# Optimization experiments

Hardware: AMD Instinct MI355X
Metric: run time of the kernel (lower is better)

Reference implementation:

```python
import jax, jax.numpy as jnp
import numpy as np

B, S, D_MODEL = 4, 1024, 1024
HEADS, D_KEY, D_VAL = 16, 64, 64


def setup_inputs() -> dict:
    key = jax.random.key(0)
    ks = jax.random.split(key, 8)
    # glorot-ish scaled params
    sk = 1.0 / np.sqrt(D_MODEL)
    X = jax.random.normal(ks[0], (B, S, D_MODEL), dtype=jnp.float32)
    Wk = jax.random.normal(ks[1], (HEADS, D_MODEL, D_KEY), dtype=jnp.float32) * sk
    Wq = jax.random.normal(ks[2], (HEADS, D_MODEL, D_KEY), dtype=jnp.float32) * sk
    Wv = jax.random.normal(ks[3], (HEADS, D_MODEL, D_VAL), dtype=jnp.float32) * sk
    bk = jnp.zeros((HEADS, D_KEY), dtype=jnp.float32)
    bq = jnp.zeros((HEADS, D_KEY), dtype=jnp.float32)
    bv = jnp.zeros((HEADS, D_VAL), dtype=jnp.float32)
    Wo = jax.random.normal(ks[4], (HEADS * D_VAL, D_MODEL), dtype=jnp.float32) * (1.0 / np.sqrt(HEADS * D_VAL))
    bo = jnp.zeros((D_MODEL,), dtype=jnp.float32)
    return {"X": X, "Wk": Wk, "bk": bk, "Wq": Wq, "bq": bq, "Wv": Wv, "bv": bv, "Wo": Wo, "bo": bo}


def reference(X, Wk, bk, Wq, bq, Wv, bv, Wo, bo):
    # Per-head projections, batched over heads (original loops in Python)
    K = jnp.einsum('bsd,hdk->bhsk', X, Wk) + bk[None, :, None, :]
    Q = jnp.einsum('bsd,hdk->bhsk', X, Wq) + bq[None, :, None, :]
    V = jnp.einsum('bsd,hdv->bhsv', X, Wv) + bv[None, :, None, :]
    d_k = K.shape[-1]
    scores = jnp.einsum('bhqk,bhsk->bhqs', Q, K) / jnp.sqrt(jnp.asarray(d_k, X.dtype))
    A = jax.nn.softmax(scores, axis=-1)           # [B,H,S,S]
    Z = jnp.einsum('bhqs,bhsv->bhqv', A, V)        # [B,H,S,Dv]
    # concat heads: [B,S,H*Dv]
    Zc = jnp.transpose(Z, (0, 2, 1, 3)).reshape(X.shape[0], X.shape[1], -1)
    # output projection + residual; dropout is identity at inference
    return Zc @ Wo + bo + X
```

## Files before the change

kernel.cpp:

```cpp
#include <hip/hip_runtime.h>
#include <hip/hip_bf16.h>

typedef __bf16 bf16x8 __attribute__((ext_vector_type(8)));
typedef float f32x4 __attribute__((ext_vector_type(4)));
typedef unsigned short u16;
typedef u16 u16x4 __attribute__((ext_vector_type(4)));
typedef u16 u16x8 __attribute__((ext_vector_type(8)));
typedef short s16x4 __attribute__((ext_vector_type(4)));

#define LDA 72

__device__ inline u16 f2bf(float f) {
    union { float f; unsigned u; } v; v.f = f;
    unsigned r = v.u + 0x7fffu + ((v.u >> 16) & 1u);
    return (u16)(r >> 16);
}

#define GLD16(g, l) __builtin_amdgcn_global_load_lds( \
    (const __attribute__((address_space(1))) unsigned int*)(g), \
    (__attribute__((address_space(3))) unsigned int*)(l), 16, 0, 0)

__global__ void k_prep(const float* __restrict__ X, u16* __restrict__ Xb,
                       const float* __restrict__ Wk, const float* __restrict__ Wq,
                       const float* __restrict__ Wv, u16* __restrict__ WT,
                       const float* __restrict__ Wo, u16* __restrict__ WoT) {
    __shared__ u16 Ls[64 * LDA];
    int u = blockIdx.x, tid = threadIdx.x;
    if (u < 4096) {
        int idx = u * 256 + tid;
        float4 v = *(const float4*)&X[(size_t)idx * 4];
        u16x4 o; o.x = f2bf(v.x); o.y = f2bf(v.y); o.z = f2bf(v.z); o.w = f2bf(v.w);
        *(u16x4*)&Xb[(size_t)idx * 4] = o;
    } else if (u < 4864) {
        int b2 = u - 4096;
        int dt = b2 & 15, h = (b2 >> 4) & 15, p = b2 >> 8;
        const float* src = (p == 0 ? Wk : p == 1 ? Wq : Wv);
        int r0 = tid >> 4, c4 = tid & 15;
        for (int j = 0; j < 4; j++) {
            int d = r0 + j * 16;
            float4 v = *(const float4*)&src[((size_t)h * 1024 + dt * 64 + d) * 64 + c4 * 4];
            u16* q = &Ls[d * LDA + c4 * 4];
            q[0] = f2bf(v.x); q[1] = f2bf(v.y); q[2] = f2bf(v.z); q[3] = f2bf(v.w);
        }
        __syncthreads();
        int nk = tid >> 2, cd = tid & 3;
        u16 tmp[16];
        for (int j = 0; j < 16; j++) tmp[j] = Ls[(cd * 16 + j) * LDA + nk];
        size_t o = ((size_t)(p * 1024 + h * 64 + nk)) * 1024 + dt * 64 + cd * 16;
        *(u16x8*)&WT[o] = *(u16x8*)&tmp[0];
        *(u16x8*)&WT[o + 8] = *(u16x8*)&tmp[8];
    } else {
        int b2 = u - 4864;
        int dt = b2 & 15, nt2 = b2 >> 4;
        int r0 = tid >> 4, c4 = tid & 15;
        for (int j = 0; j < 4; j++) {
            int d = r0 + j * 16;
            float4 v = *(const float4*)&Wo[(size_t)(dt * 64 + d) * 1024 + nt2 * 64 + c4 * 4];
            u16* q = &Ls[d * LDA + c4 * 4];
            q[0] = f2bf(v.x); q[1] = f2bf(v.y); q[2] = f2bf(v.z); q[3] = f2bf(v.w);
        }
        __syncthreads();
        int nr = tid >> 2, cd = tid & 3;
        u16 tmp[16];
        for (int j = 0; j < 16; j++) tmp[j] = Ls[(cd * 16 + j) * LDA + nr];
        size_t o = ((size_t)(nt2 * 64 + nr)) * 1024 + dt * 64 + cd * 16;
        *(u16x8*)&WoT[o] = *(u16x8*)&tmp[0];
        *(u16x8*)&WoT[o + 8] = *(u16x8*)&tmp[8];
    }
}

__global__ __launch_bounds__(256, 3) void k_qkv(
    const u16* __restrict__ Xb, const u16* __restrict__ WT,
    const float* __restrict__ bk, const float* __restrict__ bq, const float* __restrict__ bv,
    u16* __restrict__ Kw, u16* __restrict__ Qw, u16* __restrict__ Vtw)
{
    __shared__ u16 As[128 * 64];
    __shared__ u16 Bs[128 * 64];
    int tid = threadIdx.x, w = tid >> 6, lane = tid & 63, quad = lane >> 4, l16 = lane & 15;
    int wm = w & 1, wn = w >> 1;
    int m0 = blockIdx.x * 128, n0 = blockIdx.y * 128;
    int rl = lane >> 3, ch = lane & 7, swch = ch ^ rl;
    const u16* Ag = Xb + (size_t)(m0 + w * 32 + rl) * 1024 + swch * 8;
    const u16* Bg = WT + (size_t)(n0 + w * 32 + rl) * 1024 + swch * 8;

    int hb = blockIdx.y * 2 + wn;
    int p = hb >> 4, hh = hb & 15;
    bool ct = (p < 2);

    f32x4 acc[4][4] = {};
    for (int k0 = 0; k0 < 1024; k0 += 64) {
        for (int i = 0; i < 4; i++) {
            GLD16(Ag + (size_t)i * 8 * 1024 + k0, &As[(w * 32 + i * 8) * 64]);
            GLD16(Bg + (size_t)i * 8 * 1024 + k0, &Bs[(w * 32 + i * 8) * 64]);
        }
        __syncthreads();
        for (int ks = 0; ks < 2; ks++) {
            bf16x8 af[4], bf[4];
            int c = (ks << 2) | quad;
            for (int mt = 0; mt < 4; mt++) {
                int row = wm * 64 + mt * 16 + l16;
                af[mt] = *(bf16x8*)&As[row * 64 + (c ^ (row & 7)) * 8];
            }
            for (int nt = 0; nt < 4; nt++) {
                int row = wn * 64 + nt * 16 + l16;
                bf[nt] = *(bf16x8*)&Bs[row * 64 + (c ^ (row & 7)) * 8];
            }
            if (ct) {
                for (int mt = 0; mt < 4; mt++)
                    for (int nt = 0; nt < 4; nt++)
                        acc[mt][nt] = __builtin_amdgcn_mfma_f32_16x16x32_bf16(bf[nt], af[mt], acc[mt][nt], 0, 0, 0);
            } else {
                for (int mt = 0; mt < 4; mt++)
                    for (int nt = 0; nt < 4; nt++)
                        acc[mt][nt] = __builtin_amdgcn_mfma_f32_16x16x32_bf16(af[mt], bf[nt], acc[mt][nt], 0, 0, 0);
            }
        }
        __syncthreads();
    }
    const float* bias = (p == 0 ? bk : p == 1 ? bq : bv) + hh * 64;
    if (ct) {
        u16* dst = (p == 0) ? Kw : Qw;
        float sc = (p == 0) ? 0.125f : 1.0f;
        for (int mt = 0; mt < 4; mt++) {
            int m = m0 + wm * 64 + mt * 16 + l16;
            int b = m >> 10, s = m & 1023;
            size_t base = ((size_t)((b << 4) + hh) * 1024 + s) * 64;
            for (int nt = 0; nt < 4; nt++) {
                float4 bb = *(const float4*)&bias[nt * 16 + quad * 4];
                u16x4 o;
                o[0] = f2bf((acc[mt][nt][0] + bb.x) * sc);
                o[1] = f2bf((acc[mt][nt][1] + bb.y) * sc);
                o[2] = f2bf((acc[mt][nt][2] + bb.z) * sc);
                o[3] = f2bf((acc[mt][nt][3] + bb.w) * sc);
                *(u16x4*)&dst[base + nt * 16 + quad * 4] = o;
            }
        }
    } else {
        for (int mt = 0; mt < 4; mt++)
            for (int nt = 0; nt < 4; nt++) {
                int nk = nt * 16 + l16;
                float bb = bias[nk];
                int mb = m0 + wm * 64 + mt * 16 + quad * 4;
                int b = mb >> 10, s = mb & 1023;
                u16x4 o;
                for (int r = 0; r < 4; r++) o[r] = f2bf(acc[mt][nt][r] + bb);
                *(u16x4*)&Vtw[((size_t)((b << 4) + hh) * 64 + nk) * 1024 + s] = o;
            }
    }
}

__global__ __launch_bounds__(512) void k_attn(
    const u16* __restrict__ Qw, const u16* __restrict__ Kw,
    const u16* __restrict__ Vtw, u16* __restrict__ Zw)
{
    __shared__ u16 Ks[2][64 * 64];
    __shared__ u16 Vs[2][64 * 64];
    int tid = threadIdx.x, w = tid >> 6, lane = tid & 63, quad = lane >> 4, l16 = lane & 15;
    int bh = blockIdx.x, q0 = blockIdx.y * 128;
    const u16* Qp = Qw + (size_t)bh * 65536;
    int rl = lane >> 3, ch = lane & 7, swch = ch ^ rl;
    const u16* Kg = Kw + (size_t)bh * 65536 + (w * 8 + rl) * 64 + swch * 8;
    const u16* Vg = Vtw + (size_t)bh * 65536 + (size_t)(w * 8 + rl) * 1024 + swch * 8;

    bf16x8 aq[2];
    for (int ks = 0; ks < 2; ks++)
        aq[ks] = *(const bf16x8*)&Qp[(size_t)(q0 + w * 16 + l16) * 64 + ks * 32 + quad * 8];

    f32x4 accT[4] = {};
    float accs_l = 0.f;

#define STAGE(st, buf) { int s0_ = (st) * 64; \
    GLD16(Kg + s0_ * 64, &Ks[buf][(w * 8) * 64]); \
    GLD16(Vg + s0_, &Vs[buf][(w * 8) * 64]); }

    STAGE(0, 0);
    for (int st = 0; st < 16; st++) {
        int buf = st & 1;
        __syncthreads();
        if (st < 15) STAGE(st + 1, buf ^ 1);
        f32x4 sacc[4] = {};
        __builtin_amdgcn_s_setprio(1);
        for (int ks = 0; ks < 2; ks++) {
            int c = (ks << 2) | quad;
            for (int nt = 0; nt < 4; nt++) {
                int row = nt * 16 + l16;
                bf16x8 kf = *(bf16x8*)&Ks[buf][row * 64 + (c ^ (row & 7)) * 8];
                sacc[nt] = __builtin_amdgcn_mfma_f32_16x16x32_bf16(kf, aq[ks], sacc[nt], 0, 0, 0);
            }
        }
        __builtin_amdgcn_s_setprio(0);
        s16x4 pb[4];
        for (int nt = 0; nt < 4; nt++)
            for (int r = 0; r < 4; r++) {
                float p = __builtin_exp2f(__builtin_fmaf(sacc[nt][r], 1.44269504f, -23.0831206f));
                accs_l += p;
                union { float f; unsigned u; } cv; cv.f = p;
                pb[nt][r] = (short)((cv.u + 0x8000u) >> 16);
            }
        __builtin_amdgcn_s_setprio(1);
        for (int nt = 0; nt < 4; nt++) {
            int sc = nt * 2 + (quad >> 1);
            for (int db = 0; db < 4; db++) {
                int row = db * 16 + l16;
                s16x4 vf = *(const s16x4*)&Vs[buf][row * 64 + ((sc ^ (row & 7)) << 3) + ((quad & 1) << 2)];
                accT[db] = __builtin_amdgcn_mfma_f32_16x16x16bf16_1k(vf, pb[nt], accT[db], 0, 0, 0);
            }
        }
        __builtin_amdgcn_s_setprio(0);
    }
#undef STAGE
    accs_l += __shfl_xor(accs_l, 16, 64);
    accs_l += __shfl_xor(accs_l, 32, 64);
    float inv = 1.f / accs_l;
    int b = bh >> 4, h = bh & 15;
    int q = q0 + w * 16 + l16;
    size_t base = ((size_t)(b * 1024 + q)) * 1024 + h * 64;
    for (int db = 0; db < 4; db++) {
        u16x4 o;
        for (int r = 0; r < 4; r++) o[r] = f2bf(accT[db][r] * inv);
        *(u16x4*)&Zw[base + db * 16 + quad * 4] = o;
    }
}

__global__ __launch_bounds__(256) void k_oproj(
    const u16* __restrict__ Zw, const u16* __restrict__ WoT, const float* __restrict__ bo,
    const float* __restrict__ X, float* __restrict__ out)
{
    __shared__ u16 As[64 * 64];
    __shared__ u16 Bs[128 * 64];
    int tid = threadIdx.x, w = tid >> 6, lane = tid & 63, quad = lane >> 4, l16 = lane & 15;
    int wm = w & 1, wn = w >> 1;
    int m0 = blockIdx.x * 64, n0 = blockIdx.y * 128;
    int rl = lane >> 3, ch = lane & 7, swch = ch ^ rl;
    const u16* Ag = Zw + (size_t)(m0 + w * 16 + rl) * 1024 + swch * 8;
    const u16* Bg = WoT + (size_t)(n0 + w * 32 + rl) * 1024 + swch * 8;

    f32x4 acc[2][4] = {};
    for (int k0 = 0; k0 < 1024; k0 += 64) {
        for (int i = 0; i < 2; i++)
            GLD16(Ag + (size_t)i * 8 * 1024 + k0, &As[(w * 16 + i * 8) * 64]);
        for (int i = 0; i < 4; i++)
            GLD16(Bg + (size_t)i * 8 * 1024 + k0, &Bs[(w * 32 + i * 8) * 64]);
        __syncthreads();
        for (int ks = 0; ks < 2; ks++) {
            bf16x8 af[2], bf[4];
            int c = (ks << 2) | quad;
            for (int mt = 0; mt < 2; mt++) {
                int row = wm * 32 + mt * 16 + l16;
                af[mt] = *(bf16x8*)&As[row * 64 + (c ^ (row & 7)) * 8];
            }
            for (int nt = 0; nt < 4; nt++) {
                int row = wn * 64 + nt * 16 + l16;
                bf[nt] = *(bf16x8*)&Bs[row * 64 + (c ^ (row & 7)) * 8];
            }
            for (int mt = 0; mt < 2; mt++)
                for (int nt = 0; nt < 4; nt++)
                    acc[mt][nt] = __builtin_amdgcn_mfma_f32_16x16x32_bf16(af[mt], bf[nt], acc[mt][nt], 0, 0, 0);
        }
        __syncthreads();
    }
    for (int mt = 0; mt < 2; mt++)
        for (int nt = 0; nt < 4; nt++) {
            int n = n0 + wn * 64 + nt * 16 + l16;
            float bb = bo[n];
            for (int r = 0; r < 4; r++) {
                int m = m0 + wm * 32 + mt * 16 + quad * 4 + r;
                out[(size_t)m * 1024 + n] = acc[mt][nt][r] + bb + X[(size_t)m * 1024 + n];
            }
        }
}

extern "C" void kernel_launch(void* const* d_in, const int* in_sizes, int n_in,
                              void* d_out, int out_size, void* d_ws, size_t ws_size,
                              hipStream_t stream) {
    const float* X  = (const float*)d_in[0];
    const float* Wk = (const float*)d_in[1];
    const float* bk = (const float*)d_in[2];
    const float* Wq = (const float*)d_in[3];
    const float* bq = (const float*)d_in[4];
    const float* Wv = (const float*)d_in[5];
    const float* bv = (const float*)d_in[6];
    const float* Wo = (const float*)d_in[7];
    const float* bo = (const float*)d_in[8];
    u16* ws = (u16*)d_ws;
    const size_t NQ = 4u * 16u * 1024u * 64u;
    u16* Qw  = ws;
    u16* Kw  = ws + NQ;
    u16* Vtw = ws + 2 * NQ;
    u16* Zw  = ws + 3 * NQ;
    u16* WT  = ws + 4 * NQ;
    u16* WoT = WT + 3 * 1048576;
    u16* Xb  = WoT + 1048576;
    float* outp = (float*)d_out;

    k_prep <<<5120, 256, 0, stream>>>(X, Xb, Wk, Wq, Wv, WT, Wo, WoT);
    k_qkv  <<<dim3(32, 24), 256, 0, stream>>>(Xb, WT, bk, bq, bv, Kw, Qw, Vtw);
    k_attn <<<dim3(64, 8), 512, 0, stream>>>(Qw, Kw, Vtw, Zw);
    k_oproj<<<dim3(64, 8), 256, 0, stream>>>(Zw, WoT, bo, X, outp);
}
```

Measured before the change: 180.8 us.

## Double-buffer LDS tiles in QKV and output-projection GEMMs

Both GEMM kernels now keep two LDS buffers and issue the global-to-LDS loads for the next k-tile before computing on the current one, with one barrier per iteration instead of two. The aim is to hide global load latency behind MFMA work. In exchange LDS use doubles (64KB per block for k_qkv), and launch bounds for k_qkv drop from 3 to 2 blocks per CU, which lowers occupancy. The single barrier before issuing the next loads into the other buffer appears to keep the scheme race-free.

```diff
diff --git a/kernel.cpp b/kernel.cpp
--- a/kernel.cpp
+++ b/kernel.cpp
@@ -69,13 +69,13 @@
     }
 }
 
-__global__ __launch_bounds__(256, 3) void k_qkv(
+__global__ __launch_bounds__(256, 2) void k_qkv(
     const u16* __restrict__ Xb, const u16* __restrict__ WT,
     const float* __restrict__ bk, const float* __restrict__ bq, const float* __restrict__ bv,
     u16* __restrict__ Kw, u16* __restrict__ Qw, u16* __restrict__ Vtw)
 {
-    __shared__ u16 As[128 * 64];
-    __shared__ u16 Bs[128 * 64];
+    __shared__ u16 As[2][128 * 64];
+    __shared__ u16 Bs[2][128 * 64];
     int tid = threadIdx.x, w = tid >> 6, lane = tid & 63, quad = lane >> 4, l16 = lane & 15;
     int wm = w & 1, wn = w >> 1;
     int m0 = blockIdx.x * 128, n0 = blockIdx.y * 128;
@@ -87,23 +87,26 @@
     int p = hb >> 4, hh = hb & 15;
     bool ct = (p < 2);
 
+#define QSTAGE(k0, b) for (int i = 0; i < 4; i++) { \
+        GLD16(Ag + (size_t)i * 8 * 1024 + (k0), &As[b][(w * 32 + i * 8) * 64]); \
+        GLD16(Bg + (size_t)i * 8 * 1024 + (k0), &Bs[b][(w * 32 + i * 8) * 64]); }
+
     f32x4 acc[4][4] = {};
-    for (int k0 = 0; k0 < 1024; k0 += 64) {
-        for (int i = 0; i < 4; i++) {
-            GLD16(Ag + (size_t)i * 8 * 1024 + k0, &As[(w * 32 + i * 8) * 64]);
-            GLD16(Bg + (size_t)i * 8 * 1024 + k0, &Bs[(w * 32 + i * 8) * 64]);
-        }
-        __syncthreads();
+    QSTAGE(0, 0);
+    for (int kk = 0; kk < 16; kk++) {
+        int buf = kk & 1;
+        __syncthreads();
+        if (kk < 15) QSTAGE((kk + 1) * 64, buf ^ 1);
         for (int ks = 0; ks < 2; ks++) {
             bf16x8 af[4], bf[4];
             int c = (ks << 2) | quad;
             for (int mt = 0; mt < 4; mt++) {
                 int row = wm * 64 + mt * 16 + l16;
-                af[mt] = *(bf16x8*)&As[row * 64 + (c ^ (row & 7)) * 8];
+                af[mt] = *(bf16x8*)&As[buf][row * 64 + (c ^ (row & 7)) * 8];
             }
             for (int nt = 0; nt < 4; nt++) {
                 int row = wn * 64 + nt * 16 + l16;
-                bf[nt] = *(bf16x8*)&Bs[row * 64 + (c ^ (row & 7)) * 8];
+                bf[nt] = *(bf16x8*)&Bs[buf][row * 64 + (c ^ (row & 7)) * 8];
             }
             if (ct) {
                 for (int mt = 0; mt < 4; mt++)
@@ -115,8 +118,8 @@
                         acc[mt][nt] = __builtin_amdgcn_mfma_f32_16x16x32_bf16(af[mt], bf[nt], acc[mt][nt], 0, 0, 0);
             }
         }
-        __syncthreads();
-    }
+    }
+#undef QSTAGE
     const float* bias = (p == 0 ? bk : p == 1 ? bq : bv) + hh * 64;
     if (ct) {
         u16* dst = (p == 0) ? Kw : Qw;
@@ -226,8 +229,8 @@
     const u16* __restrict__ Zw, const u16* __restrict__ WoT, const float* __restrict__ bo,
     const float* __restrict__ X, float* __restrict__ out)
 {
-    __shared__ u16 As[64 * 64];
-    __shared__ u16 Bs[128 * 64];
+    __shared__ u16 As[2][64 * 64];
+    __shared__ u16 Bs[2][128 * 64];
     int tid = threadIdx.x, w = tid >> 6, lane = tid & 63, quad = lane >> 4, l16 = lane & 15;
     int wm = w & 1, wn = w >> 1;
     int m0 = blockIdx.x * 64, n0 = blockIdx.y * 128;
@@ -235,30 +238,35 @@
     const u16* Ag = Zw + (size_t)(m0 + w * 16 + rl) * 1024 + swch * 8;
     const u16* Bg = WoT + (size_t)(n0 + w * 32 + rl) * 1024 + swch * 8;
 
+#define OSTAGE(k0, b) { \
+    for (int i = 0; i < 2; i++) \
+        GLD16(Ag + (size_t)i * 8 * 1024 + (k0), &As[b][(w * 16 + i * 8) * 64]); \
+    for (int i = 0; i < 4; i++) \
+        GLD16(Bg + (size_t)i * 8 * 1024 + (k0), &Bs[b][(w * 32 + i * 8) * 64]); }
+
     f32x4 acc[2][4] = {};
-    for (int k0 = 0; k0 < 1024; k0 += 64) {
-        for (int i = 0; i < 2; i++)
-            GLD16(Ag + (size_t)i * 8 * 1024 + k0, &As[(w * 16 + i * 8) * 64]);
-        for (int i = 0; i < 4; i++)
-            GLD16(Bg + (size_t)i * 8 * 1024 + k0, &Bs[(w * 32 + i * 8) * 64]);
-        __syncthreads();
+    OSTAGE(0, 0);
+    for (int kk = 0; kk < 16; kk++) {
+        int buf = kk & 1;
+        __syncthreads();
+        if (kk < 15) OSTAGE((kk + 1) * 64, buf ^ 1);
         for (int ks = 0; ks < 2; ks++) {
             bf16x8 af[2], bf[4];
             int c = (ks << 2) | quad;
             for (int mt = 0; mt < 2; mt++) {
                 int row = wm * 32 + mt * 16 + l16;
-                af[mt] = *(bf16x8*)&As[row * 64 + (c ^ (row & 7)) * 8];
+                af[mt] = *(bf16x8*)&As[buf][row * 64 + (c ^ (row & 7)) * 8];
             }
             for (int nt = 0; nt < 4; nt++) {
                 int row = wn * 64 + nt * 16 + l16;
-                bf[nt] = *(bf16x8*)&Bs[row * 64 + (c ^ (row & 7)) * 8];
+                bf[nt] = *(bf16x8*)&Bs[buf][row * 64 + (c ^ (row & 7)) * 8];
             }
             for (int mt = 0; mt < 2; mt++)
                 for (int nt = 0; nt < 4; nt++)
                     acc[mt][nt] = __builtin_amdgcn_mfma_f32_16x16x32_bf16(af[mt], bf[nt], acc[mt][nt], 0, 0, 0);
         }
-        __syncthreads();
-    }
+    }
+#undef OSTAGE
     for (int mt = 0; mt < 2; mt++)
         for (int nt = 0; nt < 4; nt++) {
             int n = n0 + wn * 64 + nt * 16 + l16;
```

After: 185.3 us. 1.02x slower.

## Load QKV GEMM operands directly from global memory, dropping LDS staging

Applied to the files above, without the earlier changes.

The QKV projection GEMM no longer stages X and weight tiles through shared memory with global_load_lds and barriers. Each wave now reads its MFMA fragments straight from global memory into registers. This removes the LDS traffic and both __syncthreads per k-step, and it drops the occupancy hint from launch_bounds. In exchange, tiles shared between waves are read from global memory more than once, and the small per-lane reads rely on caches to keep bandwidth reasonable.

```diff
diff --git a/kernel.cpp b/kernel.cpp
--- a/kernel.cpp
+++ b/kernel.cpp
@@ -69,53 +69,49 @@
     }
 }
 
-__global__ __launch_bounds__(256, 3) void k_qkv(
+__global__ __launch_bounds__(256) void k_qkv(
     const u16* __restrict__ Xb, const u16* __restrict__ WT,
     const float* __restrict__ bk, const float* __restrict__ bq, const float* __restrict__ bv,
     u16* __restrict__ Kw, u16* __restrict__ Qw, u16* __restrict__ Vtw)
 {
-    __shared__ u16 As[128 * 64];
-    __shared__ u16 Bs[128 * 64];
     int tid = threadIdx.x, w = tid >> 6, lane = tid & 63, quad = lane >> 4, l16 = lane & 15;
     int wm = w & 1, wn = w >> 1;
     int m0 = blockIdx.x * 128, n0 = blockIdx.y * 128;
-    int rl = lane >> 3, ch = lane & 7, swch = ch ^ rl;
-    const u16* Ag = Xb + (size_t)(m0 + w * 32 + rl) * 1024 + swch * 8;
-    const u16* Bg = WT + (size_t)(n0 + w * 32 + rl) * 1024 + swch * 8;
 
     int hb = blockIdx.y * 2 + wn;
     int p = hb >> 4, hh = hb & 15;
     bool ct = (p < 2);
 
+    const u16* Ap = Xb + (size_t)(m0 + wm * 64 + l16) * 1024 + quad * 8;
+    const u16* Bp = WT + (size_t)(n0 + wn * 64 + l16) * 1024 + quad * 8;
+
     f32x4 acc[4][4] = {};
+    #pragma unroll 1
     for (int k0 = 0; k0 < 1024; k0 += 64) {
-        for (int i = 0; i < 4; i++) {
-            GLD16(Ag + (size_t)i * 8 * 1024 + k0, &As[(w * 32 + i * 8) * 64]);
-            GLD16(Bg + (size_t)i * 8 * 1024 + k0, &Bs[(w * 32 + i * 8) * 64]);
-        }
-        __syncthreads();
+        #pragma unroll
         for (int ks = 0; ks < 2; ks++) {
             bf16x8 af[4], bf[4];
-            int c = (ks << 2) | quad;
-            for (int mt = 0; mt < 4; mt++) {
-                int row = wm * 64 + mt * 16 + l16;
-                af[mt] = *(bf16x8*)&As[row * 64 + (c ^ (row & 7)) * 8];
-            }
-            for (int nt = 0; nt < 4; nt++) {
-                int row = wn * 64 + nt * 16 + l16;
-                bf[nt] = *(bf16x8*)&Bs[row * 64 + (c ^ (row & 7)) * 8];
-            }
+            int kc = k0 + ks * 32;
+            #pragma unroll
+            for (int mt = 0; mt < 4; mt++)
+                af[mt] = *(const bf16x8*)&Ap[(size_t)mt * 16384 + kc];
+            #pragma unroll
+            for (int nt = 0; nt < 4; nt++)
+                bf[nt] = *(const bf16x8*)&Bp[(size_t)nt * 16384 + kc];
             if (ct) {
+                #pragma unroll
                 for (int mt = 0; mt < 4; mt++)
+                    #pragma unroll
                     for (int nt = 0; nt < 4; nt++)
                         acc[mt][nt] = __builtin_amdgcn_mfma_f32_16x16x32_bf16(bf[nt], af[mt], acc[mt][nt], 0, 0, 0);
             } else {
+                #pragma unroll
                 for (int mt = 0; mt < 4; mt++)
+                    #pragma unroll
                     for (int nt = 0; nt < 4; nt++)
                         acc[mt][nt] = __builtin_amdgcn_mfma_f32_16x16x32_bf16(af[mt], bf[nt], acc[mt][nt], 0, 0, 0);
             }
         }
-        __syncthreads();
     }
     const float* bias = (p == 0 ? bk : p == 1 ? bq : bv) + hh * 64;
     if (ct) {
```

After: 234.9 us. 29.9% more time.

## Double-buffer LDS tiles in QKV projection GEMM to overlap loads with MFMA

Applied to the files above, without the earlier changes.

The QKV projection kernel now uses two LDS buffers for the A and B tiles. It issues the global-to-LDS loads for the next K-step before computing on the current one, and waits with explicit vmcnt counts and raw barriers. The goal is to hide global load latency behind MFMA work instead of stalling on a full sync each iteration. LDS use doubles to 64KB per block and the occupancy hint of 3 is removed, so fewer blocks may be resident per CU.

```diff
diff --git a/kernel.cpp b/kernel.cpp
--- a/kernel.cpp
+++ b/kernel.cpp
@@ -69,13 +69,13 @@
     }
 }
 
-__global__ __launch_bounds__(256, 3) void k_qkv(
+__global__ __launch_bounds__(256) void k_qkv(
     const u16* __restrict__ Xb, const u16* __restrict__ WT,
     const float* __restrict__ bk, const float* __restrict__ bq, const float* __restrict__ bv,
     u16* __restrict__ Kw, u16* __restrict__ Qw, u16* __restrict__ Vtw)
 {
-    __shared__ u16 As[128 * 64];
-    __shared__ u16 Bs[128 * 64];
+    __shared__ u16 As[2][128 * 64];
+    __shared__ u16 Bs[2][128 * 64];
     int tid = threadIdx.x, w = tid >> 6, lane = tid & 63, quad = lane >> 4, l16 = lane & 15;
     int wm = w & 1, wn = w >> 1;
     int m0 = blockIdx.x * 128, n0 = blockIdx.y * 128;
@@ -87,23 +87,29 @@
     int p = hb >> 4, hh = hb & 15;
     bool ct = (p < 2);
 
+#define QSTAGE(k0, b) for (int i = 0; i < 4; i++) { \
+        GLD16(Ag + (size_t)i * 8 * 1024 + (k0), &As[b][(w * 32 + i * 8) * 64]); \
+        GLD16(Bg + (size_t)i * 8 * 1024 + (k0), &Bs[b][(w * 32 + i * 8) * 64]); }
+#define RBAR { __builtin_amdgcn_sched_barrier(0); __builtin_amdgcn_s_barrier(); __builtin_amdgcn_sched_barrier(0); }
+#define VMCN(n) asm volatile("s_waitcnt vmcnt(" #n ")" ::: "memory")
+
     f32x4 acc[4][4] = {};
-    for (int k0 = 0; k0 < 1024; k0 += 64) {
-        for (int i = 0; i < 4; i++) {
-            GLD16(Ag + (size_t)i * 8 * 1024 + k0, &As[(w * 32 + i * 8) * 64]);
-            GLD16(Bg + (size_t)i * 8 * 1024 + k0, &Bs[(w * 32 + i * 8) * 64]);
-        }
-        __syncthreads();
+    QSTAGE(0, 0);
+    for (int kk = 0; kk < 16; kk++) {
+        int buf = kk & 1;
+        if (kk < 15) { QSTAGE((kk + 1) * 64, buf ^ 1); VMCN(8); }
+        else VMCN(0);
+        RBAR;
         for (int ks = 0; ks < 2; ks++) {
             bf16x8 af[4], bf[4];
             int c = (ks << 2) | quad;
             for (int mt = 0; mt < 4; mt++) {
                 int row = wm * 64 + mt * 16 + l16;
-                af[mt] = *(bf16x8*)&As[row * 64 + (c ^ (row & 7)) * 8];
+                af[mt] = *(bf16x8*)&As[buf][row * 64 + (c ^ (row & 7)) * 8];
             }
             for (int nt = 0; nt < 4; nt++) {
                 int row = wn * 64 + nt * 16 + l16;
-                bf[nt] = *(bf16x8*)&Bs[row * 64 + (c ^ (row & 7)) * 8];
+                bf[nt] = *(bf16x8*)&Bs[buf][row * 64 + (c ^ (row & 7)) * 8];
             }
             if (ct) {
                 for (int mt = 0; mt < 4; mt++)
@@ -115,8 +121,11 @@
                         acc[mt][nt] = __builtin_amdgcn_mfma_f32_16x16x32_bf16(af[mt], bf[nt], acc[mt][nt], 0, 0, 0);
             }
         }
-        __syncthreads();
-    }
+        RBAR;
+    }
+#undef QSTAGE
+#undef RBAR
+#undef VMCN
     const float* bias = (p == 0 ? bk : p == 1 ? bq : bv) + hh * 64;
     if (ct) {
         u16* dst = (p == 0) ? Kw : Qw;
```

After: 183.9 us. Within noise of the previous version (+1.8%).
